# Optimization experiments

Hardware: AMD Instinct MI355X
Metric: run time of the kernel (lower is better)

The kernel has to match this reference:

```python
import jax, jax.numpy as jnp
import numpy as np

DIM = 256
HEADS = 8
DHEAD = 32          # dim // 8
WIN = 128           # attn_window
NBLOCKS = 4
FF_INNER = int(DIM * 4 * 2 / 3)  # 682
SCALE = DHEAD ** -0.5


def layernorm(x, g, b):
    mu = jnp.mean(x, axis=-1, keepdims=True)
    var = jnp.mean((x - mu) ** 2, axis=-1, keepdims=True)
    return (x - mu) * jax.lax.rsqrt(var + 1e-5) * g + b


def look_around(x):
    # x: (b, h, nw, w, d) -> (b, h, nw, 3w, d); prev/current/next window, zero-padded ends
    nw = x.shape[2]
    p = jnp.pad(x, ((0, 0), (0, 0), (1, 1), (0, 0), (0, 0)))
    return jnp.concatenate([p[:, :, i:i + nw] for i in range(3)], axis=3)


def key_mask(mask):
    # mask: (b, n) bool -> (b, nw, 3w) validity of look-around keys
    b, n = mask.shape
    nw = n // WIN
    mb = mask.reshape(b, nw, WIN)
    p = jnp.pad(mb, ((0, 0), (1, 1), (0, 0)), constant_values=False)
    return jnp.concatenate([p[:, i:i + nw] for i in range(3)], axis=-1)


def local_mha(x, kmask, ln_g, ln_b, qkv_w, out_w):
    b, n, _ = x.shape
    nw = n // WIN
    xn = layernorm(x, ln_g, ln_b)
    qkv = jnp.einsum('bnd,ed->bne', xn, qkv_w)           # (b, n, 3*h*dh)
    qkv = qkv.reshape(b, nw, WIN, 3, HEADS, DHEAD)
    q, k, v = [jnp.transpose(qkv[:, :, :, i], (0, 3, 1, 2, 4)) for i in range(3)]  # (b,h,nw,w,dh)
    kk = look_around(k)                                   # (b,h,nw,3w,dh)
    vv = look_around(v)
    sim = jnp.einsum('bhnid,bhnjd->bhnij', q, kk) * SCALE  # (b,h,nw,w,3w)
    neg = -jnp.finfo(sim.dtype).max
    sim = jnp.where(kmask[:, None, :, None, :], sim, neg)
    attn = jax.nn.softmax(sim, axis=-1)
    out = jnp.einsum('bhnij,bhnjd->bhnid', attn, vv)      # (b,h,nw,w,dh)
    out = jnp.transpose(out, (0, 2, 3, 1, 4)).reshape(b, n, HEADS * DHEAD)
    return jnp.einsum('bne,de->bnd', out, out_w)


def geglu_ff(x, ln_g, ln_b, w1, w2):
    xn = layernorm(x, ln_g, ln_b)
    h = jnp.einsum('bnd,ed->bne', xn, w1)                 # (b, n, 2*FF_INNER)
    a, g = jnp.split(h, 2, axis=-1)
    y = a * jax.nn.gelu(g, approximate=False)             # exact GELU like torch
    return jnp.einsum('bne,de->bnd', y, w2)


def setup_inputs() -> dict:
    key = jax.random.key(0)
    ks = jax.random.split(key, 8)
    B, N = 8, 4096
    s = 0.02
    return {
        'x': jax.random.normal(ks[0], (B, N, DIM), dtype=jnp.float32),
        'mask': jnp.ones((B, N), dtype=bool),
        'ln1_g': jnp.ones((NBLOCKS, DIM), jnp.float32),
        'ln1_b': jnp.zeros((NBLOCKS, DIM), jnp.float32),
        'qkv_w': jax.random.normal(ks[1], (NBLOCKS, 3 * HEADS * DHEAD, DIM), jnp.float32) * s,
        'out_w': jax.random.normal(ks[2], (NBLOCKS, DIM, HEADS * DHEAD), jnp.float32) * s,
        'ln2_g': jnp.ones((NBLOCKS, DIM), jnp.float32),
        'ln2_b': jnp.zeros((NBLOCKS, DIM), jnp.float32),
        'ff_w1': jax.random.normal(ks[3], (NBLOCKS, 2 * FF_INNER, DIM), jnp.float32) * s,
        'ff_w2': jax.random.normal(ks[4], (NBLOCKS, DIM, FF_INNER), jnp.float32) * s,
    }


def reference(x, mask, ln1_g, ln1_b, qkv_w, out_w, ln2_g, ln2_b, ff_w1, ff_w2):
    kmask = key_mask(mask)
    for i in range(NBLOCKS):
        x = local_mha(x, kmask, ln1_g[i], ln1_b[i], qkv_w[i], out_w[i]) + x
        x = geglu_ff(x, ln2_g[i], ln2_b[i], ff_w1[i], ff_w2[i]) + x
    return x
```

## Files before the change

kernel.cpp:

```cpp
#include <hip/hip_runtime.h>


#define DIM 256
#define DHEAD 32
#define NWIN 32
#define SEQ 4096
#define TOKENS 32768
#define FFP 704
#define ATT_SCALE_LOG2E 0.25501818642228136f

typedef __attribute__((ext_vector_type(4))) float f32x4;
typedef __attribute__((ext_vector_type(4))) short s16x4;
typedef __attribute__((ext_vector_type(8))) short s16x8;
typedef __attribute__((ext_vector_type(4))) _Float16 f16x4;
typedef __attribute__((ext_vector_type(8))) _Float16 f16x8;

__device__ __forceinline__ short f2bf(float f) {
  unsigned int u = __float_as_uint(f);
  u += 0x7fffu + ((u >> 16) & 1u);
  return (short)(u >> 16);
}

__device__ __forceinline__ float fast_exp2(float x) {
#if __has_builtin(__builtin_amdgcn_exp2f)
  return __builtin_amdgcn_exp2f(x);
#else
  return __expf(x * 0.6931471805599453f);
#endif
}

__device__ __forceinline__ float gelu_exact(float g) {
  return 0.5f * g * (1.0f + erff(g * 0.70710678118654752440f));
}

__device__ __forceinline__ void gl_lds16(const short* g, short* l) {
  __builtin_amdgcn_global_load_lds(
      (const __attribute__((address_space(1))) void*)g,
      (__attribute__((address_space(3))) void*)l, 16, 0, 0);
}

__global__ void __launch_bounds__(256)
copy_ln(const float* __restrict__ x0, const float* __restrict__ gw,
        const float* __restrict__ bw, float* __restrict__ x, short* __restrict__ xn) {
  const int row = blockIdx.x * 4 + (threadIdx.x >> 6);
  const int lane = threadIdx.x & 63;
  const f32x4 v = *(const f32x4*)(x0 + (size_t)row * DIM + lane * 4);
  *(f32x4*)(x + (size_t)row * DIM + lane * 4) = v;
  float s = v[0] + v[1] + v[2] + v[3];
  float s2 = v[0]*v[0] + v[1]*v[1] + v[2]*v[2] + v[3]*v[3];
#pragma unroll
  for (int off = 32; off > 0; off >>= 1) {
    s  += __shfl_xor(s, off, 64);
    s2 += __shfl_xor(s2, off, 64);
  }
  const float mu = s * (1.0f / DIM);
  const float var = s2 * (1.0f / DIM) - mu * mu;
  const float rstd = rsqrtf(var + 1e-5f);
  const f32x4 gv = *(const f32x4*)(gw + lane * 4);
  const f32x4 bv = *(const f32x4*)(bw + lane * 4);
  s16x4 o;
#pragma unroll
  for (int j = 0; j < 4; ++j) o[j] = f2bf((v[j] - mu) * rstd * gv[j] + bv[j]);
  *(s16x4*)(xn + (size_t)row * DIM + lane * 4) = o;
}

template<int K, bool DO_LN>
__global__ void __launch_bounds__(512)
gemm_res_ln(const short* __restrict__ A, const short* __restrict__ W,
            float* __restrict__ x, const float* __restrict__ lng,
            const float* __restrict__ lnb, short* __restrict__ xn) {
  __shared__ short As[128 * 32];
  __shared__ short Bs[256 * 32];
  const int tid = threadIdx.x;
  const int lane = tid & 63;
  const int w = tid >> 6;
  const int ln16 = lane & 15;
  const int quad = lane >> 4;
  const int m_blk = blockIdx.x * 128;
  const int m0w = (w & 1) * 64;
  const int n0w = (w >> 1) * 64;
  const int srow = lane >> 2;
  const int scol = (lane & 3) * 8;

  const short* sg[3];
  short* dg[3];
#pragma unroll
  for (int i = 0; i < 3; ++i) {
    const int grp = w + i * 8;
    if (grp < 8) {
      sg[i] = A + (size_t)(m_blk + grp * 16 + srow) * K + scol;
      dg[i] = As + grp * 512;
    } else {
      const int gb = grp - 8;
      sg[i] = W + (size_t)(gb * 16 + srow) * K + scol;
      dg[i] = Bs + gb * 512;
    }
  }

  f32x4 acc[4][4] = {};
  for (int kb = 0; kb < K; kb += 32) {
#pragma unroll
    for (int i = 0; i < 3; ++i) gl_lds16(sg[i] + kb, dg[i]);
    __syncthreads();
    s16x8 af[4], bf[4];
#pragma unroll
    for (int mt = 0; mt < 4; ++mt)
      af[mt] = *(const s16x8*)(As + (m0w + mt * 16 + ln16) * 32 + quad * 8);
#pragma unroll
    for (int nt = 0; nt < 4; ++nt)
      bf[nt] = *(const s16x8*)(Bs + (n0w + nt * 16 + ln16) * 32 + quad * 8);
#pragma unroll
    for (int mt = 0; mt < 4; ++mt)
#pragma unroll
      for (int nt = 0; nt < 4; ++nt)
        acc[mt][nt] = __builtin_amdgcn_mfma_f32_16x16x32_bf16(af[mt], bf[nt], acc[mt][nt], 0, 0, 0);
    __syncthreads();
  }

#pragma unroll
  for (int mt = 0; mt < 4; ++mt)
#pragma unroll
    for (int nt = 0; nt < 4; ++nt)
#pragma unroll
      for (int r = 0; r < 4; ++r) {
        const size_t idx = (size_t)(m_blk + m0w + mt * 16 + quad * 4 + r) * DIM
                           + n0w + nt * 16 + ln16;
        const float v = x[idx] + acc[mt][nt][r];
        acc[mt][nt][r] = v;
        x[idx] = v;
      }

  if (DO_LN) {
    float2* red = (float2*)As;
#pragma unroll
    for (int mt = 0; mt < 4; ++mt)
#pragma unroll
      for (int r = 0; r < 4; ++r) {
        float s = 0.f, s2 = 0.f;
#pragma unroll
        for (int nt = 0; nt < 4; ++nt) {
          const float v = acc[mt][nt][r];
          s += v; s2 += v * v;
        }
#pragma unroll
        for (int off = 1; off < 16; off <<= 1) {
          s  += __shfl_xor(s, off, 64);
          s2 += __shfl_xor(s2, off, 64);
        }
        if (ln16 == 0)
          red[(m0w + mt * 16 + quad * 4 + r) * 4 + (w >> 1)] = float2{s, s2};
      }
    __syncthreads();

    float gv[4], bv[4];
#pragma unroll
    for (int nt = 0; nt < 4; ++nt) {
      gv[nt] = lng[n0w + nt * 16 + ln16];
      bv[nt] = lnb[n0w + nt * 16 + ln16];
    }
#pragma unroll
    for (int mt = 0; mt < 4; ++mt)
#pragma unroll
      for (int r = 0; r < 4; ++r) {
        const int row = m0w + mt * 16 + quad * 4 + r;
        const float2 t0 = red[row * 4 + 0];
        const float2 t1 = red[row * 4 + 1];
        const float2 t2 = red[row * 4 + 2];
        const float2 t3 = red[row * 4 + 3];
        const float s  = (t0.x + t1.x) + (t2.x + t3.x);
        const float s2 = (t0.y + t1.y) + (t2.y + t3.y);
        const float mu = s * (1.0f / DIM);
        const float var = s2 * (1.0f / DIM) - mu * mu;
        const float rstd = rsqrtf(var + 1e-5f);
#pragma unroll
        for (int nt = 0; nt < 4; ++nt)
          xn[(size_t)(m_blk + row) * DIM + n0w + nt * 16 + ln16] =
              f2bf((acc[mt][nt][r] - mu) * rstd * gv[nt] + bv[nt]);
      }
  }
}

__global__ void __launch_bounds__(256)
gemm_qkv(const short* __restrict__ A, const short* __restrict__ W,
         short* __restrict__ qh, short* __restrict__ kh, _Float16* __restrict__ vp) {
  __shared__ short As[128 * 32];
  __shared__ short Bs[128 * 32];
  const int tid = threadIdx.x;
  const int lane = tid & 63;
  const int w = tid >> 6;
  const int ln16 = lane & 15;
  const int quad = lane >> 4;
  const int m_blk = blockIdx.x * 128;
  const int n_blk = blockIdx.y * 128;

  const int srow = lane >> 2;
  const int scol = (lane & 3) * 8;
  const short* Ag0 = A + (size_t)(m_blk + w * 32 + srow) * DIM + scol;
  const short* Ag1 = Ag0 + (size_t)16 * DIM;
  const short* Wg0 = W + (size_t)(n_blk + w * 32 + srow) * DIM + scol;
  const short* Wg1 = Wg0 + (size_t)16 * DIM;
  short* Al0 = As + w * 1024;
  short* Al1 = As + w * 1024 + 512;
  short* Bl0 = Bs + w * 1024;
  short* Bl1 = Bs + w * 1024 + 512;

  const int m0w = (w & 1) * 64;
  const int n0w = (w >> 1) * 64;
  f32x4 acc[4][4] = {};

  for (int kb = 0; kb < DIM; kb += 32) {
    gl_lds16(Ag0 + kb, Al0);
    gl_lds16(Ag1 + kb, Al1);
    gl_lds16(Wg0 + kb, Bl0);
    gl_lds16(Wg1 + kb, Bl1);
    __syncthreads();
    s16x8 af[4], bf[4];
#pragma unroll
    for (int mt = 0; mt < 4; ++mt)
      af[mt] = *(const s16x8*)(As + (m0w + mt * 16 + ln16) * 32 + quad * 8);
#pragma unroll
    for (int nt = 0; nt < 4; ++nt)
      bf[nt] = *(const s16x8*)(Bs + (n0w + nt * 16 + ln16) * 32 + quad * 8);
#pragma unroll
    for (int mt = 0; mt < 4; ++mt)
#pragma unroll
      for (int nt = 0; nt < 4; ++nt)
        acc[mt][nt] = __builtin_amdgcn_mfma_f32_16x16x32_bf16(af[mt], bf[nt], acc[mt][nt], 0, 0, 0);
    __syncthreads();
  }

#pragma unroll
  for (int mt = 0; mt < 4; ++mt) {
    const int m = m_blk + m0w + mt * 16 + quad * 4;
    const int bb = m >> 12;
    const int n = m & 4095;
#pragma unroll
    for (int nt = 0; nt < 4; ++nt) {
      const int f = n_blk + n0w + nt * 16;
      if (f < 512) {
        const int ff = f & 255;
        short* dst = (f < 256 ? qh : kh)
                     + ((size_t)(bb * 8 + (ff >> 5)) * SEQ + n) * 32 + (ff & 16) + ln16;
#pragma unroll
        for (int r = 0; r < 4; ++r) dst[r * 32] = f2bf(acc[mt][nt][r]);
      } else {
        const int ff = f - 512;
        const int h = ff >> 5;
        const int d = (ff & 16) + ln16;
        const int within = n & 31;
        const int pos = (n & ~31) + ((within & 12) << 1) + ((within >> 4) << 2);
        f16x4 o;
#pragma unroll
        for (int r = 0; r < 4; ++r) o[r] = (_Float16)acc[mt][nt][r];
        *(f16x4*)(vp + ((size_t)(bb * 8 + h) * 32 + d) * SEQ + pos) = o;
      }
    }
  }
}

__global__ void __launch_bounds__(256)
gemm_geglu128(const short* __restrict__ A, const short* __restrict__ W,
              short* __restrict__ y) {
  __shared__ short As[128 * 32];
  __shared__ short Bs[2 * 64 * 32];
  const int tid = threadIdx.x;
  const int lane = tid & 63;
  const int w = tid >> 6;
  const int ln16 = lane & 15;
  const int quad = lane >> 4;
  const int m_blk = blockIdx.x * 128;
  const int n0 = blockIdx.y * 64;

  const int srow = lane >> 2;
  const int scol = (lane & 3) * 8;
  const short* Ag0 = A + (size_t)(m_blk + w * 32 + srow) * DIM + scol;
  const short* Ag1 = Ag0 + (size_t)16 * DIM;
  const int gid0 = w * 2;
  const int half0 = gid0 >> 2, r16_0 = gid0 & 3;
  const int gid1 = w * 2 + 1;
  const int half1 = gid1 >> 2, r16_1 = gid1 & 3;
  const short* Wg0 = W + (size_t)(half0 * FFP + n0 + r16_0 * 16 + srow) * DIM + scol;
  const short* Wg1 = W + (size_t)(half1 * FFP + n0 + r16_1 * 16 + srow) * DIM + scol;
  short* Al0 = As + w * 1024;
  short* Al1 = As + w * 1024 + 512;
  short* Bl0 = Bs + half0 * 2048 + r16_0 * 512;
  short* Bl1 = Bs + half1 * 2048 + r16_1 * 512;

  const int m0w = (w & 1) * 64;
  const int n0w = (w >> 1) * 32;
  f32x4 acc[2][4][2] = {};

  for (int kb = 0; kb < DIM; kb += 32) {
    gl_lds16(Ag0 + kb, Al0);
    gl_lds16(Ag1 + kb, Al1);
    gl_lds16(Wg0 + kb, Bl0);
    gl_lds16(Wg1 + kb, Bl1);
    __syncthreads();
    s16x8 af[4], ba[2], bg[2];
#pragma unroll
    for (int mt = 0; mt < 4; ++mt)
      af[mt] = *(const s16x8*)(As + (m0w + mt * 16 + ln16) * 32 + quad * 8);
#pragma unroll
    for (int nt = 0; nt < 2; ++nt) {
      ba[nt] = *(const s16x8*)(Bs + (n0w + nt * 16 + ln16) * 32 + quad * 8);
      bg[nt] = *(const s16x8*)(Bs + 2048 + (n0w + nt * 16 + ln16) * 32 + quad * 8);
    }
#pragma unroll
    for (int mt = 0; mt < 4; ++mt)
#pragma unroll
      for (int nt = 0; nt < 2; ++nt) {
        acc[0][mt][nt] = __builtin_amdgcn_mfma_f32_16x16x32_bf16(af[mt], ba[nt], acc[0][mt][nt], 0, 0, 0);
        acc[1][mt][nt] = __builtin_amdgcn_mfma_f32_16x16x32_bf16(af[mt], bg[nt], acc[1][mt][nt], 0, 0, 0);
      }
    __syncthreads();
  }

#pragma unroll
  for (int mt = 0; mt < 4; ++mt)
#pragma unroll
    for (int nt = 0; nt < 2; ++nt)
#pragma unroll
      for (int r = 0; r < 4; ++r)
        y[(size_t)(m_blk + m0w + mt * 16 + quad * 4 + r) * FFP
          + n0 + n0w + nt * 16 + ln16] =
            f2bf(acc[0][mt][nt][r] * gelu_exact(acc[1][mt][nt][r]));
}

__global__ void __launch_bounds__(256)
attn_kernel(const short* __restrict__ qh, const short* __restrict__ kh,
            const _Float16* __restrict__ vp, short* __restrict__ out) {
  const int blk = blockIdx.x;
  const int lane = threadIdx.x & 63;
  const int wid = threadIdx.x >> 6;
  const int ln16 = lane & 15;
  const int quad = lane >> 4;

  const int w = (blk & 15) * 2 + (wid >> 1);
  const int h = (blk >> 4) & 7;
  const int b = blk >> 7;
  const int plane = b * 8 + h;
  const int tok0 = w * 128 + (wid & 1) * 64;
  const int ktok = w * 128 - 128;
  const int c0 = (w == 0) ? 4 : 0;
  const int c1 = (w == NWIN - 1) ? 8 : 12;

  const short* qp = qh + ((size_t)plane * SEQ + tok0) * 32;
  s16x8 qf[4];
#pragma unroll
  for (int qi = 0; qi < 4; ++qi)
    qf[qi] = *(const s16x8*)(qp + (qi * 16 + ln16) * 32 + quad * 8);

  const short* kp = kh + ((size_t)plane * SEQ + ktok) * 32;
  const _Float16* vb = vp + ((size_t)plane * 32 + ln16) * SEQ + ktok;

  float lsum[4] = {0.f, 0.f, 0.f, 0.f};
  f32x4 ot[4][2] = {};

  s16x8 kc0 = *(const s16x8*)(kp + (c0 * 32 + ln16) * 32 + quad * 8);
  s16x8 kc1 = *(const s16x8*)(kp + (c0 * 32 + 16 + ln16) * 32 + quad * 8);
  f16x8 vc0 = *(const f16x8*)(vb + c0 * 32 + quad * 8);
  f16x8 vc1 = *(const f16x8*)(vb + (size_t)16 * SEQ + c0 * 32 + quad * 8);

  for (int c = c0; c < c1; ++c) {
    const int cn = (c + 1 < c1) ? c + 1 : c;
    s16x8 kn0 = *(const s16x8*)(kp + (cn * 32 + ln16) * 32 + quad * 8);
    s16x8 kn1 = *(const s16x8*)(kp + (cn * 32 + 16 + ln16) * 32 + quad * 8);
    f16x8 vn0 = *(const f16x8*)(vb + cn * 32 + quad * 8);
    f16x8 vn1 = *(const f16x8*)(vb + (size_t)16 * SEQ + cn * 32 + quad * 8);

    const f16x4 v00 = __builtin_shufflevector(vc0, vc0, 0, 1, 2, 3);
    const f16x4 v10 = __builtin_shufflevector(vc0, vc0, 4, 5, 6, 7);
    const f16x4 v01 = __builtin_shufflevector(vc1, vc1, 0, 1, 2, 3);
    const f16x4 v11 = __builtin_shufflevector(vc1, vc1, 4, 5, 6, 7);

#pragma unroll
    for (int qi = 0; qi < 4; ++qi) {
      const f32x4 z = {0.f, 0.f, 0.f, 0.f};
      f32x4 st0 = __builtin_amdgcn_mfma_f32_16x16x32_bf16(kc0, qf[qi], z, 0, 0, 0);
      f32x4 st1 = __builtin_amdgcn_mfma_f32_16x16x32_bf16(kc1, qf[qi], z, 0, 0, 0);
      float p[8];
#pragma unroll
      for (int r = 0; r < 4; ++r) {
        p[r]     = fast_exp2(st0[r] * ATT_SCALE_LOG2E);
        p[4 + r] = fast_exp2(st1[r] * ATT_SCALE_LOG2E);
      }
      lsum[qi] += ((p[0] + p[1]) + (p[2] + p[3])) + ((p[4] + p[5]) + (p[6] + p[7]));
      f16x4 pa, pb;
#pragma unroll
      for (int r = 0; r < 4; ++r) { pa[r] = (_Float16)p[r]; pb[r] = (_Float16)p[4 + r]; }
      ot[qi][0] = __builtin_amdgcn_mfma_f32_16x16x16f16(pa, v00, ot[qi][0], 0, 0, 0);
      ot[qi][1] = __builtin_amdgcn_mfma_f32_16x16x16f16(pa, v01, ot[qi][1], 0, 0, 0);
      ot[qi][0] = __builtin_amdgcn_mfma_f32_16x16x16f16(pb, v10, ot[qi][0], 0, 0, 0);
      ot[qi][1] = __builtin_amdgcn_mfma_f32_16x16x16f16(pb, v11, ot[qi][1], 0, 0, 0);
    }
    kc0 = kn0; kc1 = kn1; vc0 = vn0; vc1 = vn1;
  }

#pragma unroll
  for (int qi = 0; qi < 4; ++qi) {
    float l = lsum[qi];
    l += __shfl_xor(l, 16, 64);
    l += __shfl_xor(l, 32, 64);
    const float inv = 1.0f / l;
#pragma unroll
    for (int dt = 0; dt < 2; ++dt)
#pragma unroll
      for (int r = 0; r < 4; ++r)
        out[(size_t)(b * SEQ + tok0 + qi * 16 + quad * 4 + r) * DIM
            + h * DHEAD + dt * 16 + ln16] = f2bf(ot[qi][dt][r] * inv);
  }
}

__global__ void cvt_all(const float* __restrict__ qkv_w, const float* __restrict__ out_w,
                        const float* __restrict__ ff_w1, const float* __restrict__ ff_w2,
                        short* __restrict__ wqkv, short* __restrict__ wout,
                        short* __restrict__ wff1, short* __restrict__ wff2) {
  int i = blockIdx.x * 256 + threadIdx.x;
  if (i < 786432) { wqkv[i] = f2bf(qkv_w[i]); return; }
  i -= 786432;
  if (i < 262144) { wout[i] = f2bf(out_w[i]); return; }
  i -= 262144;
  if (i < 1441792) {
    const int c = i & 255;
    const int rl = i >> 8;
    const int l = rl / 1408;
    const int r = rl - l * 1408;
    const int half = r / FFP;
    const int rr = r - half * FFP;
    const float v = (rr < 682) ? ff_w1[((size_t)(l * 1364 + half * 682 + rr)) * 256 + c] : 0.0f;
    wff1[i] = f2bf(v);
    return;
  }
  i -= 1441792;
  if (i < 720896) {
    const int c = i % FFP;
    const int t = i / FFP;
    const float v = (c < 682) ? ff_w2[(size_t)t * 682 + c] : 0.0f;
    wff2[i] = f2bf(v);
  }
}

extern "C" void kernel_launch(void* const* d_in, const int* in_sizes, int n_in,
                              void* d_out, int out_size, void* d_ws, size_t ws_size,
                              hipStream_t stream) {
  const float* x0    = (const float*)d_in[0];
  const float* ln1_g = (const float*)d_in[2];
  const float* ln1_b = (const float*)d_in[3];
  const float* qkv_w = (const float*)d_in[4];
  const float* out_w = (const float*)d_in[5];
  const float* ln2_g = (const float*)d_in[6];
  const float* ln2_b = (const float*)d_in[7];
  const float* ff_w1 = (const float*)d_in[8];
  const float* ff_w2 = (const float*)d_in[9];
  float* x = (float*)d_out;

  char* ws = (char*)d_ws;
  short* wqkv = (short*)(ws);
  short* wout = (short*)(ws + 1572864);
  short* wff1 = (short*)(ws + 2097152);
  short* wff2 = (short*)(ws + 4980736);
  short* xn   = (short*)(ws + 6422528);
  short*    qhb = (short*)(ws + 23199744);
  short*    khb = (short*)(ws + 23199744 + 16777216);
  _Float16* vpb = (_Float16*)(ws + 23199744 + 33554432);
  short*    yb  = (short*)(ws + 23199744);

  copy_ln<<<8192, 256, 0, stream>>>(x0, ln1_g, ln1_b, x, xn);
  cvt_all<<<12544, 256, 0, stream>>>(qkv_w, out_w, ff_w1, ff_w2, wqkv, wout, wff1, wff2);

  for (int l = 0; l < 4; ++l) {
    gemm_qkv<<<dim3(256, 6), 256, 0, stream>>>(
        xn, wqkv + (size_t)l * 768 * DIM, qhb, khb, vpb);
    attn_kernel<<<1024, 256, 0, stream>>>(qhb, khb, vpb, xn);
    gemm_res_ln<256, true><<<256, 512, 0, stream>>>(
        xn, wout + (size_t)l * DIM * DIM, x,
        ln2_g + l * DIM, ln2_b + l * DIM, xn);
    gemm_geglu128<<<dim3(256, 11), 256, 0, stream>>>(
        xn, wff1 + (size_t)l * 2 * FFP * DIM, yb);
    if (l < 3)
      gemm_res_ln<FFP, true><<<256, 512, 0, stream>>>(
          yb, wff2 + (size_t)l * DIM * FFP, x,
          ln1_g + (l + 1) * DIM, ln1_b + (l + 1) * DIM, xn);
    else
      gemm_res_ln<FFP, false><<<256, 512, 0, stream>>>(
          yb, wff2 + (size_t)l * DIM * FFP, x, nullptr, nullptr, nullptr);
  }
}
```

Baseline: 778.3 us.

## Double GEMM K-tile to 64 with XOR-swizzled LDS layout

The three MFMA GEMM kernels (residual+LN, QKV, GEGLU) now stage 64-wide K slices per iteration instead of 32, which halves the number of barrier pairs per tile. The LDS rows are stored with an XOR swizzle (8-element groups permuted by row&7) so the fragment reads avoid bank conflicts. The cost is doubled LDS use per block, which may reduce occupancy, plus more registers for the two-half fragment arrays.

```diff
diff --git a/kernel.cpp b/kernel.cpp
--- a/kernel.cpp
+++ b/kernel.cpp
@@ -37,6 +37,10 @@
   __builtin_amdgcn_global_load_lds(
       (const __attribute__((address_space(1))) void*)g,
       (__attribute__((address_space(3))) void*)l, 16, 0, 0);
+}
+
+__device__ __forceinline__ s16x8 fragld(const short* lds, int row, int g) {
+  return *(const s16x8*)(lds + row * 64 + ((g ^ (row & 7)) << 3));
 }
 
 __global__ void __launch_bounds__(256)
@@ -69,8 +73,8 @@
 gemm_res_ln(const short* __restrict__ A, const short* __restrict__ W,
             float* __restrict__ x, const float* __restrict__ lng,
             const float* __restrict__ lnb, short* __restrict__ xn) {
-  __shared__ short As[128 * 32];
-  __shared__ short Bs[256 * 32];
+  __shared__ short As[128 * 64];
+  __shared__ short Bs[256 * 64];
   const int tid = threadIdx.x;
   const int lane = tid & 63;
   const int w = tid >> 6;
@@ -79,41 +83,46 @@
   const int m_blk = blockIdx.x * 128;
   const int m0w = (w & 1) * 64;
   const int n0w = (w >> 1) * 64;
-  const int srow = lane >> 2;
-  const int scol = (lane & 3) * 8;
-
-  const short* sg[3];
-  short* dg[3];
-#pragma unroll
-  for (int i = 0; i < 3; ++i) {
+  const int srow = lane >> 3;
+  const int swz = (lane & 7) ^ srow;
+
+  const short* sg[6];
+  short* dg[6];
+#pragma unroll
+  for (int i = 0; i < 6; ++i) {
     const int grp = w + i * 8;
-    if (grp < 8) {
-      sg[i] = A + (size_t)(m_blk + grp * 16 + srow) * K + scol;
+    if (grp < 16) {
+      sg[i] = A + (size_t)(m_blk + grp * 8 + srow) * K + swz * 8;
       dg[i] = As + grp * 512;
     } else {
-      const int gb = grp - 8;
-      sg[i] = W + (size_t)(gb * 16 + srow) * K + scol;
+      const int gb = grp - 16;
+      sg[i] = W + (size_t)(gb * 8 + srow) * K + swz * 8;
       dg[i] = Bs + gb * 512;
     }
   }
 
   f32x4 acc[4][4] = {};
-  for (int kb = 0; kb < K; kb += 32) {
-#pragma unroll
-    for (int i = 0; i < 3; ++i) gl_lds16(sg[i] + kb, dg[i]);
-    __syncthreads();
-    s16x8 af[4], bf[4];
-#pragma unroll
-    for (int mt = 0; mt < 4; ++mt)
-      af[mt] = *(const s16x8*)(As + (m0w + mt * 16 + ln16) * 32 + quad * 8);
-#pragma unroll
-    for (int nt = 0; nt < 4; ++nt)
-      bf[nt] = *(const s16x8*)(Bs + (n0w + nt * 16 + ln16) * 32 + quad * 8);
-#pragma unroll
-    for (int mt = 0; mt < 4; ++mt)
+  for (int kb = 0; kb < K; kb += 64) {
+#pragma unroll
+    for (int i = 0; i < 6; ++i) gl_lds16(sg[i] + kb, dg[i]);
+    __syncthreads();
+    s16x8 af[2][4], bf[2][4];
+#pragma unroll
+    for (int kh = 0; kh < 2; ++kh) {
+#pragma unroll
+      for (int mt = 0; mt < 4; ++mt)
+        af[kh][mt] = fragld(As, m0w + mt * 16 + ln16, kh * 4 + quad);
 #pragma unroll
       for (int nt = 0; nt < 4; ++nt)
-        acc[mt][nt] = __builtin_amdgcn_mfma_f32_16x16x32_bf16(af[mt], bf[nt], acc[mt][nt], 0, 0, 0);
+        bf[kh][nt] = fragld(Bs, n0w + nt * 16 + ln16, kh * 4 + quad);
+    }
+#pragma unroll
+    for (int kh = 0; kh < 2; ++kh)
+#pragma unroll
+      for (int mt = 0; mt < 4; ++mt)
+#pragma unroll
+        for (int nt = 0; nt < 4; ++nt)
+          acc[mt][nt] = __builtin_amdgcn_mfma_f32_16x16x32_bf16(af[kh][mt], bf[kh][nt], acc[mt][nt], 0, 0, 0);
     __syncthreads();
   }
 
@@ -182,9 +191,9 @@
 
 __global__ void __launch_bounds__(256)
 gemm_qkv(const short* __restrict__ A, const short* __restrict__ W,
-         short* __restrict__ qh, short* __restrict__ kh, _Float16* __restrict__ vp) {
-  __shared__ short As[128 * 32];
-  __shared__ short Bs[128 * 32];
+         short* __restrict__ qh, short* __restrict__ kh_, _Float16* __restrict__ vp) {
+  __shared__ short As[128 * 64];
+  __shared__ short Bs[128 * 64];
   const int tid = threadIdx.x;
   const int lane = tid & 63;
   const int w = tid >> 6;
@@ -192,40 +201,48 @@
   const int quad = lane >> 4;
   const int m_blk = blockIdx.x * 128;
   const int n_blk = blockIdx.y * 128;
-
-  const int srow = lane >> 2;
-  const int scol = (lane & 3) * 8;
-  const short* Ag0 = A + (size_t)(m_blk + w * 32 + srow) * DIM + scol;
-  const short* Ag1 = Ag0 + (size_t)16 * DIM;
-  const short* Wg0 = W + (size_t)(n_blk + w * 32 + srow) * DIM + scol;
-  const short* Wg1 = Wg0 + (size_t)16 * DIM;
-  short* Al0 = As + w * 1024;
-  short* Al1 = As + w * 1024 + 512;
-  short* Bl0 = Bs + w * 1024;
-  short* Bl1 = Bs + w * 1024 + 512;
-
   const int m0w = (w & 1) * 64;
   const int n0w = (w >> 1) * 64;
+  const int srow = lane >> 3;
+  const int swz = (lane & 7) ^ srow;
+
+  const short* sg[8];
+  short* dg[8];
+#pragma unroll
+  for (int i = 0; i < 8; ++i) {
+    const int grp = w + i * 4;
+    if (grp < 16) {
+      sg[i] = A + (size_t)(m_blk + grp * 8 + srow) * DIM + swz * 8;
+      dg[i] = As + grp * 512;
+    } else {
+      const int gb = grp - 16;
+      sg[i] = W + (size_t)(n_blk + gb * 8 + srow) * DIM + swz * 8;
+      dg[i] = Bs + gb * 512;
+    }
+  }
+
   f32x4 acc[4][4] = {};
-
-  for (int kb = 0; kb < DIM; kb += 32) {
-    gl_lds16(Ag0 + kb, Al0);
-    gl_lds16(Ag1 + kb, Al1);
-    gl_lds16(Wg0 + kb, Bl0);
-    gl_lds16(Wg1 + kb, Bl1);
-    __syncthreads();
-    s16x8 af[4], bf[4];
-#pragma unroll
-    for (int mt = 0; mt < 4; ++mt)
-      af[mt] = *(const s16x8*)(As + (m0w + mt * 16 + ln16) * 32 + quad * 8);
-#pragma unroll
-    for (int nt = 0; nt < 4; ++nt)
-      bf[nt] = *(const s16x8*)(Bs + (n0w + nt * 16 + ln16) * 32 + quad * 8);
-#pragma unroll
-    for (int mt = 0; mt < 4; ++mt)
+  for (int kb = 0; kb < DIM; kb += 64) {
+#pragma unroll
+    for (int i = 0; i < 8; ++i) gl_lds16(sg[i] + kb, dg[i]);
+    __syncthreads();
+    s16x8 af[2][4], bf[2][4];
+#pragma unroll
+    for (int kh = 0; kh < 2; ++kh) {
+#pragma unroll
+      for (int mt = 0; mt < 4; ++mt)
+        af[kh][mt] = fragld(As, m0w + mt * 16 + ln16, kh * 4 + quad);
 #pragma unroll
       for (int nt = 0; nt < 4; ++nt)
-        acc[mt][nt] = __builtin_amdgcn_mfma_f32_16x16x32_bf16(af[mt], bf[nt], acc[mt][nt], 0, 0, 0);
+        bf[kh][nt] = fragld(Bs, n0w + nt * 16 + ln16, kh * 4 + quad);
+    }
+#pragma unroll
+    for (int kh = 0; kh < 2; ++kh)
+#pragma unroll
+      for (int mt = 0; mt < 4; ++mt)
+#pragma unroll
+        for (int nt = 0; nt < 4; ++nt)
+          acc[mt][nt] = __builtin_amdgcn_mfma_f32_16x16x32_bf16(af[kh][mt], bf[kh][nt], acc[mt][nt], 0, 0, 0);
     __syncthreads();
   }
 
@@ -239,7 +256,7 @@
       const int f = n_blk + n0w + nt * 16;
       if (f < 512) {
         const int ff = f & 255;
-        short* dst = (f < 256 ? qh : kh)
+        short* dst = (f < 256 ? qh : kh_)
                      + ((size_t)(bb * 8 + (ff >> 5)) * SEQ + n) * 32 + (ff & 16) + ln16;
 #pragma unroll
         for (int r = 0; r < 4; ++r) dst[r * 32] = f2bf(acc[mt][nt][r]);
@@ -261,8 +278,8 @@
 __global__ void __launch_bounds__(256)
 gemm_geglu128(const short* __restrict__ A, const short* __restrict__ W,
               short* __restrict__ y) {
-  __shared__ short As[128 * 32];
-  __shared__ short Bs[2 * 64 * 32];
+  __shared__ short As[128 * 64];
+  __shared__ short Bs[128 * 64];
   const int tid = threadIdx.x;
   const int lane = tid & 63;
   const int w = tid >> 6;
@@ -270,48 +287,53 @@
   const int quad = lane >> 4;
   const int m_blk = blockIdx.x * 128;
   const int n0 = blockIdx.y * 64;
-
-  const int srow = lane >> 2;
-  const int scol = (lane & 3) * 8;
-  const short* Ag0 = A + (size_t)(m_blk + w * 32 + srow) * DIM + scol;
-  const short* Ag1 = Ag0 + (size_t)16 * DIM;
-  const int gid0 = w * 2;
-  const int half0 = gid0 >> 2, r16_0 = gid0 & 3;
-  const int gid1 = w * 2 + 1;
-  const int half1 = gid1 >> 2, r16_1 = gid1 & 3;
-  const short* Wg0 = W + (size_t)(half0 * FFP + n0 + r16_0 * 16 + srow) * DIM + scol;
-  const short* Wg1 = W + (size_t)(half1 * FFP + n0 + r16_1 * 16 + srow) * DIM + scol;
-  short* Al0 = As + w * 1024;
-  short* Al1 = As + w * 1024 + 512;
-  short* Bl0 = Bs + half0 * 2048 + r16_0 * 512;
-  short* Bl1 = Bs + half1 * 2048 + r16_1 * 512;
-
   const int m0w = (w & 1) * 64;
   const int n0w = (w >> 1) * 32;
+  const int srow = lane >> 3;
+  const int swz = (lane & 7) ^ srow;
+
+  const short* sg[8];
+  short* dg[8];
+#pragma unroll
+  for (int i = 0; i < 8; ++i) {
+    const int grp = w + i * 4;
+    if (grp < 16) {
+      sg[i] = A + (size_t)(m_blk + grp * 8 + srow) * DIM + swz * 8;
+      dg[i] = As + grp * 512;
+    } else {
+      const int gb = grp - 16;
+      const int half = gb >> 3;
+      sg[i] = W + (size_t)(half * FFP + n0 + (gb & 7) * 8 + srow) * DIM + swz * 8;
+      dg[i] = Bs + gb * 512;
+    }
+  }
+
   f32x4 acc[2][4][2] = {};
-
-  for (int kb = 0; kb < DIM; kb += 32) {
-    gl_lds16(Ag0 + kb, Al0);
-    gl_lds16(Ag1 + kb, Al1);
-    gl_lds16(Wg0 + kb, Bl0);
-    gl_lds16(Wg1 + kb, Bl1);
-    __syncthreads();
-    s16x8 af[4], ba[2], bg[2];
-#pragma unroll
-    for (int mt = 0; mt < 4; ++mt)
-      af[mt] = *(const s16x8*)(As + (m0w + mt * 16 + ln16) * 32 + quad * 8);
-#pragma unroll
-    for (int nt = 0; nt < 2; ++nt) {
-      ba[nt] = *(const s16x8*)(Bs + (n0w + nt * 16 + ln16) * 32 + quad * 8);
-      bg[nt] = *(const s16x8*)(Bs + 2048 + (n0w + nt * 16 + ln16) * 32 + quad * 8);
-    }
-#pragma unroll
-    for (int mt = 0; mt < 4; ++mt)
+  for (int kb = 0; kb < DIM; kb += 64) {
+#pragma unroll
+    for (int i = 0; i < 8; ++i) gl_lds16(sg[i] + kb, dg[i]);
+    __syncthreads();
+    s16x8 af[2][4], ba[2][2], bg[2][2];
+#pragma unroll
+    for (int kh = 0; kh < 2; ++kh) {
+#pragma unroll
+      for (int mt = 0; mt < 4; ++mt)
+        af[kh][mt] = fragld(As, m0w + mt * 16 + ln16, kh * 4 + quad);
 #pragma unroll
       for (int nt = 0; nt < 2; ++nt) {
-        acc[0][mt][nt] = __builtin_amdgcn_mfma_f32_16x16x32_bf16(af[mt], ba[nt], acc[0][mt][nt], 0, 0, 0);
-        acc[1][mt][nt] = __builtin_amdgcn_mfma_f32_16x16x32_bf16(af[mt], bg[nt], acc[1][mt][nt], 0, 0, 0);
+        ba[kh][nt] = fragld(Bs, n0w + nt * 16 + ln16, kh * 4 + quad);
+        bg[kh][nt] = fragld(Bs, 64 + n0w + nt * 16 + ln16, kh * 4 + quad);
       }
+    }
+#pragma unroll
+    for (int kh = 0; kh < 2; ++kh)
+#pragma unroll
+      for (int mt = 0; mt < 4; ++mt)
+#pragma unroll
+        for (int nt = 0; nt < 2; ++nt) {
+          acc[0][mt][nt] = __builtin_amdgcn_mfma_f32_16x16x32_bf16(af[kh][mt], ba[kh][nt], acc[0][mt][nt], 0, 0, 0);
+          acc[1][mt][nt] = __builtin_amdgcn_mfma_f32_16x16x32_bf16(af[kh][mt], bg[kh][nt], acc[1][mt][nt], 0, 0, 0);
+        }
     __syncthreads();
   }
 
```

New measurement: 695.9 us. -10.6%, faster.
